# Performance work log

Hardware: AMD Instinct MI355X
Metric: run time of the kernel (lower is better)

## Reference

```python
import jax, jax.numpy as jnp
import numpy as np
from jax.scipy.special import logsumexp

IN_FEATURES = 1024
N_CLASSES = 50257
CUTOFFS = [4000, 20000, N_CLASSES]  # includes final n_classes, as in the module
SHORTLIST = CUTOFFS[0]
N_CLUSTERS = len(CUTOFFS)
N = 8192


def setup_inputs() -> dict:
    key = jax.random.key(0)
    k1, k2, k3, k4, k5, k6 = jax.random.split(key, 6)
    inp = {
        "input": jax.random.normal(k1, (N, IN_FEATURES), dtype=jnp.float32),
        "target": jax.random.randint(k2, (N,), 0, N_CLASSES, dtype=jnp.int64)
        if jax.config.jax_enable_x64 else jax.random.randint(k2, (N,), 0, N_CLASSES, dtype=jnp.int32),
        # learned parameters
        "weight": jax.random.normal(k3, (N_CLASSES, IN_FEATURES), dtype=jnp.float32) * 0.02,
        "bias": jnp.zeros((N_CLASSES,), dtype=jnp.float32),
        "tail_vectors": jax.random.normal(k4, (N_CLUSTERS - 1, IN_FEATURES), dtype=jnp.float32) * 0.02,
        "tail_bias": jnp.zeros((N_CLUSTERS - 1,), dtype=jnp.float32),
    }
    return inp


def reference(input, target, weight, bias, tail_vectors, tail_bias):
    cutoff_values = [0] + CUTOFFS  # [0, 4000, 20000, 50257]

    # head = shortlist classes + one logit per tail cluster
    head_weight = jnp.concatenate([weight[:SHORTLIST], tail_vectors], axis=0)
    head_bias = jnp.concatenate([bias[:SHORTLIST], tail_bias], axis=0)
    head_logits = input @ head_weight.T + head_bias              # [N, shortlist + n_clusters-1]
    head_logprob = jax.nn.log_softmax(head_logits, axis=1)

    # which cluster each target falls in: 0 = shortlist, 1.. = tails
    boundaries = jnp.asarray(CUTOFFS[:-1])                        # [4000, 20000]
    cluster_id = jnp.searchsorted(boundaries, target, side="right")  # [N]

    # index into head distribution: target itself for shortlist, else cluster logit slot
    gather_inds = jnp.where(cluster_id == 0, target, SHORTLIST + cluster_id - 1)
    head_term = jnp.take_along_axis(head_logprob, gather_inds[:, None], axis=1)[:, 0]

    # per-row target logit against the full table (only used for tail rows)
    target_logit = jnp.sum(input * weight[target], axis=-1) + bias[target]  # [N]

    # tail clusters: within-cluster log-prob of the target = logit - logsumexp(cluster logits)
    tail_term = jnp.zeros_like(head_term)
    for i in range(1, N_CLUSTERS):
        lo, hi = cutoff_values[i], cutoff_values[i + 1]
        cluster_logits = input @ weight[lo:hi].T + bias[lo:hi]    # [N, hi-lo]
        lse = logsumexp(cluster_logits, axis=1)                   # [N]
        tail_term = jnp.where(cluster_id == i, target_logit - lse, tail_term)

    output = head_term + tail_term                                # [N] log-probs of targets
    loss = jnp.mean(-output)
    return output, loss
```

## Files before the change

### kernel.cpp

```cpp
#include <hip/hip_runtime.h>
#include <stddef.h>
#include <stdint.h>

#define IN_F      1024
#define SHORTLIST 4000
#define C1_LO     4000
#define C1_HI     20000
#define C2_HI     50257
#define NROWS     8192

#define WS_CNT1   0
#define WS_CNT2   1
#define WS_LOSS   2
#define WS_RL1    4
#define WS_RL2    (4 + 8192)
#define WS_SEH    (4 + 2*8192)
#define WS_SET    (WS_SEH + 8192)
#define WS_CAP    (WS_SET + 8192)
#define WS_WORDS  (WS_CAP + 8192)

#define WBF_OFF   (262144)
#define XBF_OFF   (WBF_OFF + 103219200)
#define XBF_BYTES ((size_t)NROWS * IN_F * 2)
#define WS_NEEDED (XBF_OFF + XBF_BYTES)

#define GRID_HEAD 512
#define GRID_T1   2048
#define GRID_T2   3840
#define GRID_ALL  (GRID_HEAD + GRID_T1 + GRID_T2)

typedef float          f32x4  __attribute__((ext_vector_type(4)));
typedef __bf16         bf16x8 __attribute__((ext_vector_type(8)));
typedef unsigned short us8    __attribute__((ext_vector_type(8)));
typedef unsigned short ushort_t;

__device__ __forceinline__ unsigned short f2bf(float f) {
    unsigned int u = __float_as_uint(f);
    u += 0x7fffu + ((u >> 16) & 1u);
    return (unsigned short)(u >> 16);
}

__device__ __forceinline__ void gl_lds16(const void* g, void* l) {
    __builtin_amdgcn_global_load_lds(
        (const __attribute__((address_space(1))) void*)g,
        (__attribute__((address_space(3))) void*)l, 16, 0, 0);
}

__global__ void init_ws_k(int* __restrict__ ws) {
    int i = blockIdx.x * 256 + threadIdx.x;
    if (i < WS_WORDS) {
        int v = (i >= WS_RL1 && i < WS_RL1 + 2*8192) ? -1 : 0;
        ws[i] = v;
    }
}

__global__ void compact_rows_k(const int* __restrict__ target, int* __restrict__ ws) {
    int row = blockIdx.x * 256 + threadIdx.x;
    if (row >= NROWS) return;
    int tg = target[row];
    if (tg >= C1_LO) {
        if (tg < C1_HI) {
            int p = atomicAdd(&ws[WS_CNT1], 1);
            ws[WS_RL1 + p] = row;
        } else {
            int p = atomicAdd(&ws[WS_CNT2], 1);
            ws[WS_RL2 + p] = row;
        }
    }
}

#define WCHUNKS ((C2_HI * IN_F) / 8)
#define XCHUNKS ((NROWS * IN_F) / 8)
__global__ void convert_bf16_k(const float* __restrict__ w_src,
                               ushort_t* __restrict__ w_dst,
                               const float* __restrict__ x_src,
                               ushort_t* __restrict__ x_dst) {
    int i = blockIdx.x * 256 + threadIdx.x;
    const float* p;
    ushort_t* d;
    if (i < WCHUNKS) { p = w_src + (size_t)i * 8; d = w_dst + (size_t)i * 8; }
    else {
        int j = i - WCHUNKS;
        if (j >= XCHUNKS) return;
        p = x_src + (size_t)j * 8; d = x_dst + (size_t)j * 8;
    }
    f32x4 x0 = *(const f32x4*)p;
    f32x4 x1 = *(const f32x4*)(p + 4);
    us8 o;
    o[0] = f2bf(x0[0]); o[1] = f2bf(x0[1]); o[2] = f2bf(x0[2]); o[3] = f2bf(x0[3]);
    o[4] = f2bf(x1[0]); o[5] = f2bf(x1[1]); o[6] = f2bf(x1[2]); o[7] = f2bf(x1[3]);
    *(us8*)d = o;
}

__launch_bounds__(256)
__global__ void gemm_lse_fused_k(const ushort_t* __restrict__ Xbf,
                                 const ushort_t* __restrict__ Wbf,
                                 const float* __restrict__ bias,
                                 const int*   __restrict__ target,
                                 int*   __restrict__ wsI,
                                 float* __restrict__ wsF)
{
    const int bid = blockIdx.x;
    int rs, cg, cbase, C, cnt;
    const int* rowlist;
    float* sumexp;
    if (bid < GRID_HEAD) {
        rs = bid & 63; cg = bid >> 6;
        cbase = 0; C = SHORTLIST; rowlist = nullptr; cnt = NROWS;
        sumexp = wsF + WS_SEH;
    } else if (bid < GRID_HEAD + GRID_T1) {
        int b = bid - GRID_HEAD;
        rs = b & 63; cg = b >> 6;
        cbase = C1_LO; C = C1_HI - C1_LO; rowlist = wsI + WS_RL1; cnt = wsI[WS_CNT1];
        sumexp = wsF + WS_SET;
    } else {
        int b = bid - (GRID_HEAD + GRID_T1);
        rs = b & 63; cg = b >> 6;
        cbase = C1_HI; C = C2_HI - C1_HI; rowlist = wsI + WS_RL2; cnt = wsI[WS_CNT2];
        sumexp = wsF + WS_SET;
    }
    const int r0 = rs * 128;
    if (r0 >= cnt) return;
    float* capture = wsF + WS_CAP;

    __shared__ ushort_t As[128 * 64];
    __shared__ ushort_t Bs[128 * 64];
    __shared__ int   orig_s[128];
    __shared__ int   tgt_s[128];
    __shared__ float part[256];

    const int tid = threadIdx.x;
    part[tid] = 0.f;
    if (tid < 128) {
        int idx  = r0 + tid;
        int orig = (idx < cnt) ? (rowlist ? rowlist[idx] : idx) : -1;
        orig_s[tid] = orig;
        tgt_s[tid]  = (orig >= 0) ? target[orig] : -1;
    }
    __syncthreads();

    const int lane = tid & 63;
    const int wave = tid >> 6;
    const int wm = wave >> 1, wn = wave & 1;
    const int q = lane >> 4, s = lane & 15;

    const int lrow  = lane >> 3;
    const int chunk = (lane & 7) ^ lrow;
    const ushort_t* aptr[4];
    ushort_t* alds[4];
    ushort_t* blds[4];
    int brow[4];
#pragma unroll
    for (int i = 0; i < 4; ++i) {
        int t  = wave * 4 + i;
        int rt = t * 8 + lrow;
        int orig = orig_s[rt]; if (orig < 0) orig = 0;
        aptr[i] = Xbf + (size_t)orig * IN_F + chunk * 8;
        alds[i] = &As[t * 512];
        blds[i] = &Bs[t * 512];
        brow[i] = rt;
    }

    int aoff[4], boff[4];
#pragma unroll
    for (int i = 0; i < 4; ++i) {
        aoff[i] = (wm * 64 + i * 16 + s) * 64;
        boff[i] = (wn * 64 + i * 16 + s) * 64;
    }
    const int slot0 = (q ^ (s & 7)) * 8;
    const int slot1 = slot0 ^ (4 * 8);

    for (int ct = 0; ct < 4; ++ct) {
        const int c0 = (cg * 4 + ct) * 128;
        if (c0 >= C) break;

        const ushort_t* bptr[4];
#pragma unroll
        for (int i = 0; i < 4; ++i) {
            int c = c0 + brow[i]; if (c >= C) c = C - 1;
            bptr[i] = Wbf + (size_t)(cbase + c) * IN_F + chunk * 8;
        }

        f32x4 acc[4][4];
#pragma unroll
        for (int mi = 0; mi < 4; ++mi)
#pragma unroll
            for (int ni = 0; ni < 4; ++ni) acc[mi][ni] = (f32x4)0.f;

        for (int k0 = 0; k0 < IN_F; k0 += 64) {
            __syncthreads();
#pragma unroll
            for (int i = 0; i < 4; ++i) {
                gl_lds16(aptr[i] + k0, alds[i]);
                gl_lds16(bptr[i] + k0, blds[i]);
            }
            __syncthreads();

#pragma unroll
            for (int ks = 0; ks < 2; ++ks) {
                const int sl = ks ? slot1 : slot0;
                bf16x8 av[4], bv[4];
#pragma unroll
                for (int i = 0; i < 4; ++i) {
                    av[i] = *(const bf16x8*)&As[aoff[i] + sl];
                    bv[i] = *(const bf16x8*)&Bs[boff[i] + sl];
                }
#pragma unroll
                for (int mi = 0; mi < 4; ++mi)
#pragma unroll
                    for (int ni = 0; ni < 4; ++ni)
                        acc[mi][ni] = __builtin_amdgcn_mfma_f32_16x16x32_bf16(
                            av[mi], bv[ni], acc[mi][ni], 0, 0, 0);
            }
        }

        float bias_v[4];
#pragma unroll
        for (int ni = 0; ni < 4; ++ni) {
            int cgl = c0 + wn * 64 + ni * 16 + s;
            bias_v[ni] = (cgl < C) ? bias[cbase + cgl] : 0.f;
        }
#pragma unroll
        for (int mi = 0; mi < 4; ++mi) {
#pragma unroll
            for (int r = 0; r < 4; ++r) {
                int rl   = wm * 64 + mi * 16 + q * 4 + r;
                int orig = orig_s[rl];
                int tg   = tgt_s[rl];
                float sum = 0.f;
#pragma unroll
                for (int ni = 0; ni < 4; ++ni) {
                    int cgl = c0 + wn * 64 + ni * 16 + s;
                    float logit = acc[mi][ni][r] + bias_v[ni];
                    bool valid = (cgl < C) && (orig >= 0);
                    float e = valid ? __expf(logit) : 0.f;
                    sum += e;
                    if (valid && (cbase + cgl == tg)) capture[orig] = logit;
                }
                sum += __shfl_xor(sum, 1, 64);
                sum += __shfl_xor(sum, 2, 64);
                sum += __shfl_xor(sum, 4, 64);
                sum += __shfl_xor(sum, 8, 64);
                if (s == 0 && orig >= 0) part[wn * 128 + rl] += sum;
            }
        }
    }

    __syncthreads();
    if (tid < 128) {
        int orig = orig_s[tid];
        if (orig >= 0) {
            float tot = part[tid] + part[128 + tid];
            atomicAdd(&sumexp[orig], tot);
        }
    }
}

__launch_bounds__(256)
__global__ void gemm_lse_k(const float* __restrict__ input,
                           const float* __restrict__ weight,
                           const float* __restrict__ bias,
                           const int*   __restrict__ target,
                           const int*   __restrict__ rowlist,
                           const int*   __restrict__ cnt_ptr,
                           int fixed_cnt,
                           int class_base, int C,
                           float* __restrict__ sumexp,
                           float* __restrict__ capture)
{
    const int cnt = cnt_ptr ? *cnt_ptr : fixed_cnt;
    const int r0  = blockIdx.x * 128;
    if (r0 >= cnt) return;
    const int c0  = blockIdx.y * 128;

    __shared__ unsigned short As[128 * 40];
    __shared__ unsigned short Bs[128 * 40];
    __shared__ int   orig_s[128];
    __shared__ int   tgt_s[128];
    __shared__ float bias_s[128];

    const int tid = threadIdx.x;
    if (tid < 128) {
        int idx  = r0 + tid;
        int orig = -1;
        if (idx < cnt) orig = rowlist ? rowlist[idx] : idx;
        orig_s[tid] = orig;
        tgt_s[tid]  = (orig >= 0) ? target[orig] : -1;
        int c = c0 + tid;
        bias_s[tid] = (c < C) ? bias[class_base + c] : 0.f;
    }

    const int lane = tid & 63;
    const int wave = tid >> 6;
    const int wm = wave >> 1, wn = wave & 1;
    const int q = lane >> 4, s = lane & 15;

    int aoff[4], boff[4];
#pragma unroll
    for (int i = 0; i < 4; ++i) {
        aoff[i] = (wm * 64 + i * 16 + s) * 40 + q * 8;
        boff[i] = (wn * 64 + i * 16 + s) * 40 + q * 8;
    }

    f32x4 acc[4][4];
#pragma unroll
    for (int mi = 0; mi < 4; ++mi)
#pragma unroll
        for (int ni = 0; ni < 4; ++ni) acc[mi][ni] = (f32x4)0.f;

    for (int k0 = 0; k0 < IN_F; k0 += 32) {
        __syncthreads();
#pragma unroll
        for (int i = 0; i < 2; ++i) {
            int sg  = tid + i * 256;
            int row = sg >> 2;
            int sk  = (sg & 3) << 3;
            {
                int orig = orig_s[row];
                float v[8];
                if (orig >= 0) {
                    const float* p = input + (size_t)orig * IN_F + k0 + sk;
                    f32x4 x0 = *(const f32x4*)p;
                    f32x4 x1 = *(const f32x4*)(p + 4);
                    v[0]=x0[0]; v[1]=x0[1]; v[2]=x0[2]; v[3]=x0[3];
                    v[4]=x1[0]; v[5]=x1[1]; v[6]=x1[2]; v[7]=x1[3];
                } else {
#pragma unroll
                    for (int j = 0; j < 8; ++j) v[j] = 0.f;
                }
                us8 o;
#pragma unroll
                for (int j = 0; j < 8; ++j) o[j] = f2bf(v[j]);
                *(us8*)&As[row * 40 + sk] = o;
            }
            {
                int c = c0 + row;
                float v[8];
                if (c < C) {
                    const float* p = weight + (size_t)(class_base + c) * IN_F + k0 + sk;
                    f32x4 x0 = *(const f32x4*)p;
                    f32x4 x1 = *(const f32x4*)(p + 4);
                    v[0]=x0[0]; v[1]=x0[1]; v[2]=x0[2]; v[3]=x0[3];
                    v[4]=x1[0]; v[5]=x1[1]; v[6]=x1[2]; v[7]=x1[3];
                } else {
#pragma unroll
                    for (int j = 0; j < 8; ++j) v[j] = 0.f;
                }
                us8 o;
#pragma unroll
                for (int j = 0; j < 8; ++j) o[j] = f2bf(v[j]);
                *(us8*)&Bs[row * 40 + sk] = o;
            }
        }
        __syncthreads();

        bf16x8 av[4], bv[4];
#pragma unroll
        for (int i = 0; i < 4; ++i) {
            av[i] = *(const bf16x8*)&As[aoff[i]];
            bv[i] = *(const bf16x8*)&Bs[boff[i]];
        }
#pragma unroll
        for (int mi = 0; mi < 4; ++mi)
#pragma unroll
            for (int ni = 0; ni < 4; ++ni)
                acc[mi][ni] = __builtin_amdgcn_mfma_f32_16x16x32_bf16(
                    av[mi], bv[ni], acc[mi][ni], 0, 0, 0);
    }

#pragma unroll
    for (int mi = 0; mi < 4; ++mi) {
#pragma unroll
        for (int r = 0; r < 4; ++r) {
            int rl   = wm * 64 + mi * 16 + q * 4 + r;
            int orig = orig_s[rl];
            int tg   = tgt_s[rl];
            float sum = 0.f;
#pragma unroll
            for (int ni = 0; ni < 4; ++ni) {
                int cl = wn * 64 + ni * 16 + s;
                int cg = c0 + cl;
                float logit = acc[mi][ni][r] + bias_s[cl];
                bool valid = (cg < C) && (orig >= 0);
                float e = valid ? __expf(logit) : 0.f;
                sum += e;
                if (valid && (class_base + cg == tg)) capture[orig] = logit;
            }
            sum += __shfl_xor(sum, 1, 64);
            sum += __shfl_xor(sum, 2, 64);
            sum += __shfl_xor(sum, 4, 64);
            sum += __shfl_xor(sum, 8, 64);
            if (s == 0 && orig >= 0) atomicAdd(&sumexp[orig], sum);
        }
    }
}

__global__ void combine_k(const float* __restrict__ input,
                          const int*   __restrict__ target,
                          const float* __restrict__ tv,
                          const float* __restrict__ tb,
                          const float* __restrict__ sumexp_head,
                          const float* __restrict__ sumexp_tail,
                          const float* __restrict__ capture,
                          float* __restrict__ out,
                          float* __restrict__ loss_accum)
{
    const int wave = threadIdx.x >> 6, lane = threadIdx.x & 63;
    const int row = blockIdx.x * 4 + wave;
    if (row >= NROWS) return;

    const float* x  = input + (size_t)row * IN_F + lane * 16;
    const float* p0 = tv + lane * 16;
    const float* p1 = tv + IN_F + lane * 16;
    float d0 = 0.f, d1 = 0.f;
#pragma unroll
    for (int i = 0; i < 16; i += 4) {
        f32x4 xv = *(const f32x4*)(x  + i);
        f32x4 a  = *(const f32x4*)(p0 + i);
        f32x4 b  = *(const f32x4*)(p1 + i);
        d0 += xv[0]*a[0] + xv[1]*a[1] + xv[2]*a[2] + xv[3]*a[3];
        d1 += xv[0]*b[0] + xv[1]*b[1] + xv[2]*b[2] + xv[3]*b[3];
    }
#pragma unroll
    for (int m = 32; m; m >>= 1) {
        d0 += __shfl_xor(d0, m, 64);
        d1 += __shfl_xor(d1, m, 64);
    }
    if (lane == 0) {
        float t0 = d0 + tb[0];
        float t1 = d1 + tb[1];
        int tg  = target[row];
        int cid = (tg < C1_LO) ? 0 : ((tg < C1_HI) ? 1 : 2);
        float se_head  = sumexp_head[row] + __expf(t0) + __expf(t1);
        float lse_head = __logf(se_head);
        float head_num = (cid == 0) ? capture[row] : ((cid == 1) ? t0 : t1);
        float o = head_num - lse_head;
        if (cid != 0) o += capture[row] - __logf(sumexp_tail[row]);
        out[row] = o;
        atomicAdd(loss_accum, o);
    }
}

__global__ void finalize_k(const float* __restrict__ loss_accum, float* __restrict__ out) {
    out[NROWS] = -loss_accum[0] * (1.0f / NROWS);
}

extern "C" void kernel_launch(void* const* d_in, const int* in_sizes, int n_in,
                              void* d_out, int out_size, void* d_ws, size_t ws_size,
                              hipStream_t stream) {
    const float* input  = (const float*)d_in[0];
    const int*   target = (const int*)  d_in[1];
    const float* weight = (const float*)d_in[2];
    const float* bias   = (const float*)d_in[3];
    const float* tv     = (const float*)d_in[4];
    const float* tb     = (const float*)d_in[5];
    float* out = (float*)d_out;
    int*   wsI = (int*)d_ws;
    float* wsF = (float*)d_ws;

    init_ws_k<<<dim3((WS_WORDS + 255) / 256), 256, 0, stream>>>(wsI);
    compact_rows_k<<<dim3(NROWS / 256), 256, 0, stream>>>(target, wsI);

    const bool fast = ws_size >= (size_t)WS_NEEDED;

    if (fast) {
        ushort_t* Wbf = (ushort_t*)((char*)d_ws + WBF_OFF);
        ushort_t* Xbf = (ushort_t*)((char*)d_ws + XBF_OFF);

        convert_bf16_k<<<dim3((WCHUNKS + XCHUNKS + 255) / 256), 256, 0, stream>>>(
            weight, Wbf, input, Xbf);

        gemm_lse_fused_k<<<dim3(GRID_ALL), 256, 0, stream>>>(
            Xbf, Wbf, bias, target, wsI, wsF);
    } else {
        gemm_lse_k<<<dim3(NROWS / 128, (SHORTLIST + 127) / 128), 256, 0, stream>>>(
            input, weight, bias, target,
            nullptr, nullptr, NROWS,
            0, SHORTLIST,
            wsF + WS_SEH, wsF + WS_CAP);
        gemm_lse_k<<<dim3(NROWS / 128, (C1_HI - C1_LO + 127) / 128), 256, 0, stream>>>(
            input, weight, bias, target,
            wsI + WS_RL1, wsI + WS_CNT1, 0,
            C1_LO, C1_HI - C1_LO,
            wsF + WS_SET, wsF + WS_CAP);
        gemm_lse_k<<<dim3(NROWS / 128, (C2_HI - C1_HI + 127) / 128), 256, 0, stream>>>(
            input, weight, bias, target,
            wsI + WS_RL2, wsI + WS_CNT2, 0,
            C1_HI, C2_HI - C1_HI,
            wsF + WS_SET, wsF + WS_CAP);
    }

    combine_k<<<dim3(NROWS / 4), 256, 0, stream>>>(
        input, target, tv, tb,
        wsF + WS_SEH, wsF + WS_SET, wsF + WS_CAP,
        out, wsF + WS_LOSS);

    finalize_k<<<1, 1, 0, stream>>>(wsF + WS_LOSS, out);
}
```

Measured before the change: 1.441 ms.

## Double-buffer LDS tiles to overlap global loads with MFMA compute

Splits the A/B shared-memory tiles into two buffers and issues the next k-slice's global-to-LDS loads before computing on the current one. The loads run across column-tile boundaries, so the first slice of the next tile is prefetched during the epilogue of the current one, and each k-step has one barrier instead of two. This targets load latency exposed between barriers, at the cost of twice the LDS per block, which may lower occupancy.

Result: slower. 1.650 ms (+14.5%).

```diff
diff --git a/kernel.cpp b/kernel.cpp
--- a/kernel.cpp
+++ b/kernel.cpp
@@ -123,8 +123,8 @@
     if (r0 >= cnt) return;
     float* capture = wsF + WS_CAP;
 
-    __shared__ ushort_t As[128 * 64];
-    __shared__ ushort_t Bs[128 * 64];
+    __shared__ ushort_t As[2][128 * 64];
+    __shared__ ushort_t Bs[2][128 * 64];
     __shared__ int   orig_s[128];
     __shared__ int   tgt_s[128];
     __shared__ float part[256];
@@ -147,18 +147,16 @@
     const int lrow  = lane >> 3;
     const int chunk = (lane & 7) ^ lrow;
     const ushort_t* aptr[4];
-    ushort_t* alds[4];
-    ushort_t* blds[4];
+    int tslot[4];
     int brow[4];
 #pragma unroll
     for (int i = 0; i < 4; ++i) {
         int t  = wave * 4 + i;
         int rt = t * 8 + lrow;
         int orig = orig_s[rt]; if (orig < 0) orig = 0;
-        aptr[i] = Xbf + (size_t)orig * IN_F + chunk * 8;
-        alds[i] = &As[t * 512];
-        blds[i] = &Bs[t * 512];
-        brow[i] = rt;
+        aptr[i]  = Xbf + (size_t)orig * IN_F + chunk * 8;
+        tslot[i] = t * 512;
+        brow[i]  = rt;
     }
 
     int aoff[4], boff[4];
@@ -170,15 +168,32 @@
     const int slot0 = (q ^ (s & 7)) * 8;
     const int slot1 = slot0 ^ (4 * 8);
 
-    for (int ct = 0; ct < 4; ++ct) {
+    int nct = (C - cg * 512 + 127) >> 7;
+    if (nct > 4) nct = 4;
+
+    const ushort_t* bptr[4];
+#pragma unroll
+    for (int i = 0; i < 4; ++i) {
+        int c = cg * 512 + brow[i]; if (c >= C) c = C - 1;
+        bptr[i] = Wbf + (size_t)(cbase + c) * IN_F + chunk * 8;
+    }
+
+#pragma unroll
+    for (int i = 0; i < 4; ++i) {
+        gl_lds16(aptr[i], &As[0][tslot[i]]);
+        gl_lds16(bptr[i], &Bs[0][tslot[i]]);
+    }
+    __syncthreads();
+
+    int pb = 0;
+    for (int ct = 0; ct < nct; ++ct) {
         const int c0 = (cg * 4 + ct) * 128;
-        if (c0 >= C) break;
-
-        const ushort_t* bptr[4];
-#pragma unroll
-        for (int i = 0; i < 4; ++i) {
-            int c = c0 + brow[i]; if (c >= C) c = C - 1;
-            bptr[i] = Wbf + (size_t)(cbase + c) * IN_F + chunk * 8;
+
+        float bias_v[4];
+#pragma unroll
+        for (int ni = 0; ni < 4; ++ni) {
+            int cgl = c0 + wn * 64 + ni * 16 + s;
+            bias_v[ni] = (cgl < C) ? bias[cbase + cgl] : 0.f;
         }
 
         f32x4 acc[4][4];
@@ -188,13 +203,28 @@
             for (int ni = 0; ni < 4; ++ni) acc[mi][ni] = (f32x4)0.f;
 
         for (int k0 = 0; k0 < IN_F; k0 += 64) {
-            __syncthreads();
-#pragma unroll
-            for (int i = 0; i < 4; ++i) {
-                gl_lds16(aptr[i] + k0, alds[i]);
-                gl_lds16(bptr[i] + k0, blds[i]);
+            const int nb = pb ^ 1;
+            const int nk = k0 + 64;
+
+            if (nk < IN_F) {
+#pragma unroll
+                for (int i = 0; i < 4; ++i) {
+                    gl_lds16(aptr[i] + nk, &As[nb][tslot[i]]);
+                    gl_lds16(bptr[i] + nk, &Bs[nb][tslot[i]]);
+                }
+            } else if (ct + 1 < nct) {
+                const int nc0 = c0 + 128;
+#pragma unroll
+                for (int i = 0; i < 4; ++i) {
+                    int c = nc0 + brow[i]; if (c >= C) c = C - 1;
+                    bptr[i] = Wbf + (size_t)(cbase + c) * IN_F + chunk * 8;
+                }
+#pragma unroll
+                for (int i = 0; i < 4; ++i) {
+                    gl_lds16(aptr[i], &As[nb][tslot[i]]);
+                    gl_lds16(bptr[i], &Bs[nb][tslot[i]]);
+                }
             }
-            __syncthreads();
 
 #pragma unroll
             for (int ks = 0; ks < 2; ++ks) {
@@ -202,8 +232,8 @@
                 bf16x8 av[4], bv[4];
 #pragma unroll
                 for (int i = 0; i < 4; ++i) {
-                    av[i] = *(const bf16x8*)&As[aoff[i] + sl];
-                    bv[i] = *(const bf16x8*)&Bs[boff[i] + sl];
+                    av[i] = *(const bf16x8*)&As[pb][aoff[i] + sl];
+                    bv[i] = *(const bf16x8*)&Bs[pb][boff[i] + sl];
                 }
 #pragma unroll
                 for (int mi = 0; mi < 4; ++mi)
@@ -212,37 +242,36 @@
                         acc[mi][ni] = __builtin_amdgcn_mfma_f32_16x16x32_bf16(
                             av[mi], bv[ni], acc[mi][ni], 0, 0, 0);
             }
-        }
-
-        float bias_v[4];
-#pragma unroll
-        for (int ni = 0; ni < 4; ++ni) {
-            int cgl = c0 + wn * 64 + ni * 16 + s;
-            bias_v[ni] = (cgl < C) ? bias[cbase + cgl] : 0.f;
-        }
-#pragma unroll
-        for (int mi = 0; mi < 4; ++mi) {
-#pragma unroll
-            for (int r = 0; r < 4; ++r) {
-                int rl   = wm * 64 + mi * 16 + q * 4 + r;
-                int orig = orig_s[rl];
-                int tg   = tgt_s[rl];
-                float sum = 0.f;
-#pragma unroll
-                for (int ni = 0; ni < 4; ++ni) {
-                    int cgl = c0 + wn * 64 + ni * 16 + s;
-                    float logit = acc[mi][ni][r] + bias_v[ni];
-                    bool valid = (cgl < C) && (orig >= 0);
-                    float e = valid ? __expf(logit) : 0.f;
-                    sum += e;
-                    if (valid && (cbase + cgl == tg)) capture[orig] = logit;
-                }
-                sum += __shfl_xor(sum, 1, 64);
-                sum += __shfl_xor(sum, 2, 64);
-                sum += __shfl_xor(sum, 4, 64);
-                sum += __shfl_xor(sum, 8, 64);
-                if (s == 0 && orig >= 0) part[wn * 128 + rl] += sum;
+
+            if (nk == IN_F) {
+#pragma unroll
+                for (int mi = 0; mi < 4; ++mi) {
+#pragma unroll
+                    for (int r = 0; r < 4; ++r) {
+                        int rl   = wm * 64 + mi * 16 + q * 4 + r;
+                        int orig = orig_s[rl];
+                        int tg   = tgt_s[rl];
+                        float sum = 0.f;
+#pragma unroll
+                        for (int ni = 0; ni < 4; ++ni) {
+                            int cgl = c0 + wn * 64 + ni * 16 + s;
+                            float logit = acc[mi][ni][r] + bias_v[ni];
+                            bool valid = (cgl < C) && (orig >= 0);
+                            float e = valid ? __expf(logit) : 0.f;
+                            sum += e;
+                            if (valid && (cbase + cgl == tg)) capture[orig] = logit;
+                        }
+                        sum += __shfl_xor(sum, 1, 64);
+                        sum += __shfl_xor(sum, 2, 64);
+                        sum += __shfl_xor(sum, 4, 64);
+                        sum += __shfl_xor(sum, 8, 64);
+                        if (s == 0 && orig >= 0) part[wn * 128 + rl] += sum;
+                    }
+                }
             }
+
+            __syncthreads();
+            pb = nb;
         }
     }
 
```
